# Optimization experiments

Measured on AMD Instinct MI355X. Metric: run time of the kernel, lower is better.

The kernel has to match this reference:

```python
import jax, jax.numpy as jnp
import numpy as np

EMBED = 768
HEADS = 12
HEAD_DIM = EMBED // HEADS
B, T = 2, 2048


def setup_inputs() -> dict:
    key = jax.random.key(0)
    ks = jax.random.split(key, 5)
    scale = 0.02
    return {
        "x": jax.random.normal(ks[0], (B, T, EMBED), dtype=jnp.float32),
        "Wq": jax.random.normal(ks[1], (HEADS, EMBED, HEAD_DIM), dtype=jnp.float32) * scale,
        "Wk": jax.random.normal(ks[2], (HEADS, EMBED, HEAD_DIM), dtype=jnp.float32) * scale,
        "Wv": jax.random.normal(ks[3], (HEADS, EMBED, HEAD_DIM), dtype=jnp.float32) * scale,
        "Wp": jax.random.normal(ks[4], (EMBED, EMBED), dtype=jnp.float32) * scale,
        "bp": jnp.zeros((EMBED,), dtype=jnp.float32),
    }


def reference(x, Wq, Wk, Wv, Wp, bp):
    # x: [B,T,E]; per-head projections batched over the head axis.
    q = jnp.einsum("bte,hed->bhtd", x, Wq)  # [B,H,T,Dh]
    k = jnp.einsum("bte,hed->bhtd", x, Wk)
    v = jnp.einsum("bte,hed->bhtd", x, Wv)
    scale = 1.0 / jnp.sqrt(jnp.asarray(HEAD_DIM, dtype=x.dtype))
    scores = jnp.einsum("bhtd,bhsd->bhts", q, k) * scale  # [B,H,T,T]
    Tlen = x.shape[1]
    causal = jnp.tril(jnp.ones((Tlen, Tlen), dtype=bool))
    scores = jnp.where(causal[None, None], scores, jnp.asarray(-jnp.inf, dtype=scores.dtype))
    attn = jax.nn.softmax(scores, axis=-1)
    out = jnp.einsum("bhts,bhsd->bhtd", attn, v)  # [B,H,T,Dh]
    # concat heads (same layout as torch.cat over per-head outputs)
    out = out.transpose(0, 2, 1, 3).reshape(x.shape[0], Tlen, HEADS * HEAD_DIM)
    return out @ Wp + bp
```

## Files before the change

### kernel.cpp

```cpp
#include <hip/hip_runtime.h>
#include <math.h>

namespace {

constexpr int E_  = 768;
constexpr int H_  = 12;
constexpr int DH_ = 64;
constexpr int T_  = 2048;
constexpr int B_  = 2;
constexpr int M_  = B_ * T_;

typedef __attribute__((ext_vector_type(8))) short bf16x8;
typedef __attribute__((ext_vector_type(4))) float f32x4;

__device__ inline ushort f2bf(float f) {
  union { float f; unsigned u; } v; v.f = f;
  unsigned u = v.u + 0x7FFFu + ((v.u >> 16) & 1u);
  return (ushort)(u >> 16);
}

__device__ __forceinline__ void gl16(const ushort* g, ushort* l) {
  __builtin_amdgcn_global_load_lds(
      (const __attribute__((address_space(1))) unsigned int*)(g),
      (__attribute__((address_space(3))) unsigned int*)(l), 16, 0, 0);
}

__global__ __launch_bounds__(256) void convert_x_k(
    const float* __restrict__ x, ushort* __restrict__ xb)
{
  const size_t i = ((size_t)blockIdx.x * 256 + threadIdx.x) * 8;
  float4 a = *(const float4*)(x + i);
  float4 b = *(const float4*)(x + i + 4);
  ushort o[8] = {f2bf(a.x), f2bf(a.y), f2bf(a.z), f2bf(a.w),
                 f2bf(b.x), f2bf(b.y), f2bf(b.z), f2bf(b.w)};
  *(bf16x8*)(xb + i) = *(bf16x8*)o;
}

__global__ __launch_bounds__(256) void transpose_w_k(
    const float* __restrict__ Wq, const float* __restrict__ Wk,
    const float* __restrict__ Wv, const float* __restrict__ Wp,
    ushort* __restrict__ Wt, ushort* __restrict__ Wpt)
{
  __shared__ float tile[64][65];
  const int bid = blockIdx.x;
  const int tid = threadIdx.x;
  const int tr = tid >> 4, tc = tid & 15;

  const float* src; ushort* dst;
  int k0, n0, sN, dK;
  if (bid < 432) {
    const int mat = bid / 144, rem = bid % 144;
    const int h = rem / 12, ktile = rem % 12;
    const float* W = (mat == 0) ? Wq : (mat == 1) ? Wk : Wv;
    src = W + (size_t)h * E_ * DH_;
    dst = Wt + (size_t)(mat * H_ + h) * DH_ * E_;
    k0 = ktile * 64; n0 = 0; sN = DH_; dK = E_;
  } else {
    const int rem = bid - 432;
    src = Wp;
    dst = Wpt;
    k0 = (rem / 12) * 64; n0 = (rem % 12) * 64; sN = E_; dK = E_;
  }

#pragma unroll
  for (int rr = 0; rr < 64; rr += 16) {
    float4 v = *(const float4*)(src + (size_t)(k0 + tr + rr) * sN + n0 + tc * 4);
    tile[tr + rr][tc * 4 + 0] = v.x;
    tile[tr + rr][tc * 4 + 1] = v.y;
    tile[tr + rr][tc * 4 + 2] = v.z;
    tile[tr + rr][tc * 4 + 3] = v.w;
  }
  __syncthreads();
#pragma unroll
  for (int rr = 0; rr < 64; rr += 16) {
    const int n = tr + rr;
    ushort4 o;
    o.x = f2bf(tile[tc * 4 + 0][n]);
    o.y = f2bf(tile[tc * 4 + 1][n]);
    o.z = f2bf(tile[tc * 4 + 2][n]);
    o.w = f2bf(tile[tc * 4 + 3][n]);
    *(ushort4*)(dst + (size_t)(n0 + n) * dK + k0 + tc * 4) = o;
  }
}

constexpr float QSCALE = 0.18033688f;

__global__ __launch_bounds__(256) void qkv_fused_k(
    const ushort* __restrict__ xb, const ushort* __restrict__ Wt,
    ushort* __restrict__ q_ws, ushort* __restrict__ k_ws, ushort* __restrict__ vt_ws)
{
  __shared__ __align__(16) ushort lds[2 * 128 * 64];
  ushort* As = lds;
  ushort* Bs = lds + 128 * 64;

  const int n0 = blockIdx.x * 128;
  const int m0 = blockIdx.y * 128;

  const int tid  = threadIdx.x;
  const int w    = tid >> 6, l = tid & 63;
  const int lrow = l & 15, lk = l >> 4;
  const int r7   = lrow & 7;

  const int srow = l >> 3;
  const int sch  = (l & 7) ^ srow;

  f32x4 acc[2][8] = {};

  for (int k0 = 0; k0 < E_; k0 += 64) {
#pragma unroll
    for (int r = 0; r < 4; ++r) {
      const int base = r * 32 + w * 8;
      gl16(xb + (size_t)(m0 + base + srow) * E_ + k0 + sch * 8, &As[base * 64]);
      gl16(Wt + (size_t)(n0 + base + srow) * E_ + k0 + sch * 8, &Bs[base * 64]);
    }
    __syncthreads();

#pragma unroll
    for (int kk = 0; kk < 2; ++kk) {
      const int cof = ((kk * 4 + lk) ^ r7) * 8;
      const bf16x8 a0 = *(const bf16x8*)&As[(w * 32 + lrow) * 64 + cof];
      const bf16x8 a1 = *(const bf16x8*)&As[(w * 32 + 16 + lrow) * 64 + cof];
#pragma unroll
      for (int nf = 0; nf < 8; ++nf) {
        const bf16x8 b = *(const bf16x8*)&Bs[(nf * 16 + lrow) * 64 + cof];
        acc[0][nf] = __builtin_amdgcn_mfma_f32_16x16x32_bf16(a0, b, acc[0][nf], 0, 0, 0);
        acc[1][nf] = __builtin_amdgcn_mfma_f32_16x16x32_bf16(a1, b, acc[1][nf], 0, 0, 0);
      }
    }
    __syncthreads();
  }

  const int b  = m0 >> 11;
  const int t0 = m0 & 2047;
  ushort* Td = lds;

#pragma unroll
  for (int half = 0; half < 2; ++half) {
    const int seg = (n0 >> 6) + half;
    const int mat = seg / H_;
    const int h   = seg - mat * H_;
    const int bh  = b * H_ + h;

    if (mat != 2) {
      const float qs = (mat == 0) ? QSCALE : 1.0f;
      ushort* outw = (mat == 0) ? q_ws : k_ws;
#pragma unroll
      for (int mi = 0; mi < 2; ++mi)
#pragma unroll
        for (int i = 0; i < 4; ++i) {
          const int t = t0 + w * 32 + mi * 16 + lk * 4 + i;
          ushort* orow = outw + ((size_t)bh * T_ + t) * DH_;
#pragma unroll
          for (int nf2 = 0; nf2 < 4; ++nf2)
            orow[nf2 * 16 + lrow] = f2bf(acc[mi][half * 4 + nf2][i] * qs);
        }
    } else {
      __syncthreads();
#pragma unroll
      for (int mi = 0; mi < 2; ++mi)
#pragma unroll
        for (int i = 0; i < 4; ++i) {
          const int tl = w * 32 + mi * 16 + lk * 4 + i;
#pragma unroll
          for (int nf2 = 0; nf2 < 4; ++nf2)
            Td[(nf2 * 16 + lrow) * 136 + tl] = f2bf(acc[mi][half * 4 + nf2][i]);
        }
      __syncthreads();
#pragma unroll
      for (int it = 0; it < 4; ++it) {
        const int c = tid + it * 256;
        const int d = c >> 4, sub = c & 15;
        *(bf16x8*)(vt_ws + ((size_t)bh * DH_ + d) * T_ + t0 + sub * 8) =
            *(const bf16x8*)&Td[d * 136 + sub * 8];
      }
    }
  }
}

__global__ __launch_bounds__(256) void attn_mfma_k(
    const ushort* __restrict__ q_ws, const ushort* __restrict__ k_ws,
    const ushort* __restrict__ vt_ws, ushort* __restrict__ o_ws)
{
  __shared__ __align__(16) ushort Ks[2][64 * 64];
  __shared__ __align__(16) ushort Vt[2][64 * 64];
  __shared__ __align__(16) ushort Pl[4][16 * 64];

  const int qt = 31 - (int)blockIdx.y;
  const int bh = blockIdx.x;
  const int q0 = qt * 64;
  const ushort* Qb  = q_ws + (size_t)bh * T_ * DH_;
  const ushort* Kb  = k_ws + (size_t)bh * T_ * DH_;
  const ushort* VTb = vt_ws + (size_t)bh * DH_ * T_;

  const int tid  = threadIdx.x;
  const int w    = tid >> 6;
  const int l    = tid & 63;
  const int lrow = l & 15;
  const int lk   = l >> 4;
  const int r7   = lrow & 7;
  const int rr   = tid >> 3;
  const int sub  = tid & 7;
  const int swc  = sub ^ (rr & 7);

  const int st0 = rr * 64 + swc * 8;
  const int st1 = (rr + 32) * 64 + swc * 8;

  int kof0[4], kof1[4];
#pragma unroll
  for (int ct = 0; ct < 4; ++ct) {
    kof0[ct] = (ct * 16 + lrow) * 64 + ((lk ^ r7) * 8);
    kof1[ct] = (ct * 16 + lrow) * 64 + (((lk + 4) ^ r7) * 8);
  }

  const ushort* Qrow = Qb + (size_t)(q0 + w * 16 + lrow) * DH_;
  const bf16x8 qa0 = *(const bf16x8*)(Qrow + lk * 8);
  const bf16x8 qa1 = *(const bf16x8*)(Qrow + lk * 8 + 32);
  const int qglob = q0 + w * 16 + lrow;

  float m_r = -INFINITY, l_r = 0.f;
  f32x4 oc[4] = {};

  ushort* Pw = &Pl[w][0];
  const int rd0 = lrow * 64 + ((lk ^ r7) * 8);
  const int rd1 = lrow * 64 + (((lk + 4) ^ r7) * 8);
  const int wrbase  = lrow * 128 + (lk & 1) * 8;
  const int wrchunk = (lk >> 1);

  bf16x8 kp0 = *(const bf16x8*)(Kb + (size_t)rr * DH_ + sub * 8);
  bf16x8 kp1 = *(const bf16x8*)(Kb + (size_t)(rr + 32) * DH_ + sub * 8);
  bf16x8 vp0 = *(const bf16x8*)(VTb + (size_t)rr * T_ + sub * 8);
  bf16x8 vp1 = *(const bf16x8*)(VTb + (size_t)(rr + 32) * T_ + sub * 8);
  *(bf16x8*)&Ks[0][st0] = kp0;
  *(bf16x8*)&Ks[0][st1] = kp1;
  *(bf16x8*)&Vt[0][st0] = vp0;
  *(bf16x8*)&Vt[0][st1] = vp1;
  __syncthreads();

  for (int kt = 0; kt <= qt; ++kt) {
    const int s0  = kt * 64;
    const int cur = kt & 1;

    if (kt < qt) {
      const int sn = s0 + 64;
      kp0 = *(const bf16x8*)(Kb + (size_t)(sn + rr) * DH_ + sub * 8);
      kp1 = *(const bf16x8*)(Kb + (size_t)(sn + rr + 32) * DH_ + sub * 8);
      vp0 = *(const bf16x8*)(VTb + (size_t)rr * T_ + sn + sub * 8);
      vp1 = *(const bf16x8*)(VTb + (size_t)(rr + 32) * T_ + sn + sub * 8);
    }

    f32x4 st[4];
#pragma unroll
    for (int ct = 0; ct < 4; ++ct) {
      const bf16x8 kb0 = *(const bf16x8*)&Ks[cur][kof0[ct]];
      const bf16x8 kb1 = *(const bf16x8*)&Ks[cur][kof1[ct]];
      f32x4 z = {0.f, 0.f, 0.f, 0.f};
      z = __builtin_amdgcn_mfma_f32_16x16x32_bf16(kb0, qa0, z, 0, 0, 0);
      st[ct] = __builtin_amdgcn_mfma_f32_16x16x32_bf16(kb1, qa1, z, 0, 0, 0);
    }

    if (kt == qt) {
#pragma unroll
      for (int ct = 0; ct < 4; ++ct)
#pragma unroll
        for (int i = 0; i < 4; ++i)
          if (s0 + ct * 16 + lk * 4 + i > qglob) st[ct][i] = -INFINITY;
    }

    float mc[4];
#pragma unroll
    for (int ct = 0; ct < 4; ++ct)
      mc[ct] = fmaxf(fmaxf(st[ct][0], st[ct][1]), fmaxf(st[ct][2], st[ct][3]));
    float mx = fmaxf(fmaxf(mc[0], mc[1]), fmaxf(mc[2], mc[3]));
    mx = fmaxf(mx, __shfl_xor(mx, 16));
    mx = fmaxf(mx, __shfl_xor(mx, 32));

    if (__any(mx > m_r + 8.f)) {
      const float mn   = fmaxf(m_r, mx);
      const float corr = exp2f(m_r - mn);
      m_r = mn;
      l_r *= corr;
#pragma unroll
      for (int i = 0; i < 4; ++i) {
        const float cr = __shfl(corr, lk * 4 + i);
#pragma unroll
        for (int ct = 0; ct < 4; ++ct) oc[ct][i] *= cr;
      }
    }

    float sc[4];
#pragma unroll
    for (int ct = 0; ct < 4; ++ct) {
#pragma unroll
      for (int i = 0; i < 4; ++i) st[ct][i] = exp2f(st[ct][i] - m_r);
      sc[ct] = (st[ct][0] + st[ct][1]) + (st[ct][2] + st[ct][3]);
    }
    float rs = (sc[0] + sc[1]) + (sc[2] + sc[3]);
    rs += __shfl_xor(rs, 16);
    rs += __shfl_xor(rs, 32);
    l_r += rs;

#pragma unroll
    for (int ct = 0; ct < 4; ++ct) {
      unsigned lo, hi;
      asm("v_cvt_pk_bf16_f32 %0, %1, %2" : "=v"(lo) : "v"(st[ct][0]), "v"(st[ct][1]));
      asm("v_cvt_pk_bf16_f32 %0, %1, %2" : "=v"(hi) : "v"(st[ct][2]), "v"(st[ct][3]));
      uint2 pk; pk.x = lo; pk.y = hi;
      const int ch = ((ct * 2 + wrchunk) ^ r7);
      *(uint2*)((char*)Pw + wrbase + ch * 16) = pk;
    }

    const bf16x8 pa0 = *(const bf16x8*)(Pw + rd0);
    const bf16x8 pa1 = *(const bf16x8*)(Pw + rd1);

#pragma unroll
    for (int ct = 0; ct < 4; ++ct) {
      const bf16x8 vb0 = *(const bf16x8*)&Vt[cur][kof0[ct]];
      const bf16x8 vb1 = *(const bf16x8*)&Vt[cur][kof1[ct]];
      oc[ct] = __builtin_amdgcn_mfma_f32_16x16x32_bf16(pa0, vb0, oc[ct], 0, 0, 0);
      oc[ct] = __builtin_amdgcn_mfma_f32_16x16x32_bf16(pa1, vb1, oc[ct], 0, 0, 0);
    }

    if (kt < qt) {
      const int nxt = cur ^ 1;
      *(bf16x8*)&Ks[nxt][st0] = kp0;
      *(bf16x8*)&Ks[nxt][st1] = kp1;
      *(bf16x8*)&Vt[nxt][st0] = vp0;
      *(bf16x8*)&Vt[nxt][st1] = vp1;
    }
    __syncthreads();
  }

  const int bb = bh / H_, hh = bh - (bh / H_) * H_;
#pragma unroll
  for (int i = 0; i < 4; ++i) {
    const float lv  = __shfl(l_r, lk * 4 + i);
    const float inv = 1.0f / lv;
    const int t = q0 + w * 16 + lk * 4 + i;
    ushort* orow = o_ws + ((size_t)bb * T_ + t) * E_ + hh * DH_;
#pragma unroll
    for (int ct = 0; ct < 4; ++ct)
      orow[ct * 16 + lrow] = f2bf(oc[ct][i] * inv);
  }
}

__global__ __launch_bounds__(256) void proj2_k(
    const ushort* __restrict__ ob, const ushort* __restrict__ Wpt,
    const float* __restrict__ bp, float* __restrict__ out)
{
  __shared__ __align__(16) ushort lds[2 * 128 * 64];
  ushort* As = lds;
  ushort* Bs = lds + 128 * 64;

  const int n0 = blockIdx.x * 128;
  const int m0 = blockIdx.y * 128;

  const int tid  = threadIdx.x;
  const int w    = tid >> 6, l = tid & 63;
  const int lrow = l & 15, lk = l >> 4;
  const int r7   = lrow & 7;
  const int srow = l >> 3;
  const int sch  = (l & 7) ^ srow;

  f32x4 acc[2][8] = {};

  for (int k0 = 0; k0 < E_; k0 += 64) {
#pragma unroll
    for (int r = 0; r < 4; ++r) {
      const int base = r * 32 + w * 8;
      gl16(ob  + (size_t)(m0 + base + srow) * E_ + k0 + sch * 8, &As[base * 64]);
      gl16(Wpt + (size_t)(n0 + base + srow) * E_ + k0 + sch * 8, &Bs[base * 64]);
    }
    __syncthreads();

#pragma unroll
    for (int kk = 0; kk < 2; ++kk) {
      const int cof = ((kk * 4 + lk) ^ r7) * 8;
      const bf16x8 a0 = *(const bf16x8*)&As[(w * 32 + lrow) * 64 + cof];
      const bf16x8 a1 = *(const bf16x8*)&As[(w * 32 + 16 + lrow) * 64 + cof];
#pragma unroll
      for (int nf = 0; nf < 8; ++nf) {
        const bf16x8 b = *(const bf16x8*)&Bs[(nf * 16 + lrow) * 64 + cof];
        acc[0][nf] = __builtin_amdgcn_mfma_f32_16x16x32_bf16(a0, b, acc[0][nf], 0, 0, 0);
        acc[1][nf] = __builtin_amdgcn_mfma_f32_16x16x32_bf16(a1, b, acc[1][nf], 0, 0, 0);
      }
    }
    __syncthreads();
  }

  float bias[8];
#pragma unroll
  for (int nf = 0; nf < 8; ++nf) bias[nf] = bp[n0 + nf * 16 + lrow];

#pragma unroll
  for (int mi = 0; mi < 2; ++mi)
#pragma unroll
    for (int i = 0; i < 4; ++i) {
      const int m = m0 + w * 32 + mi * 16 + lk * 4 + i;
      float* orow = out + (size_t)m * E_ + n0;
#pragma unroll
      for (int nf = 0; nf < 8; ++nf)
        orow[nf * 16 + lrow] = acc[mi][nf][i] + bias[nf];
    }
}

}

extern "C" void kernel_launch(void* const* d_in, const int* in_sizes, int n_in,
                              void* d_out, int out_size, void* d_ws, size_t ws_size,
                              hipStream_t stream) {
  const float* x  = (const float*)d_in[0];
  const float* Wq = (const float*)d_in[1];
  const float* Wk = (const float*)d_in[2];
  const float* Wv = (const float*)d_in[3];
  const float* Wp = (const float*)d_in[4];
  const float* bp = (const float*)d_in[5];
  float* out = (float*)d_out;

  const size_t nx  = (size_t)M_ * E_;
  const size_t nwt = (size_t)3 * H_ * DH_ * E_;
  const size_t nwp = (size_t)E_ * E_;
  const size_t per = (size_t)B_ * H_ * T_ * DH_;

  ushort* xb    = (ushort*)d_ws;
  ushort* Wt    = xb + nx;
  ushort* Wpt   = Wt + nwt;
  ushort* q_ws  = Wpt + nwp;
  ushort* k_ws  = q_ws + per;
  ushort* vt_ws = k_ws + per;
  ushort* o_b   = vt_ws + per;

  convert_x_k<<<dim3((int)(nx / (256 * 8))), 256, 0, stream>>>(x, xb);
  transpose_w_k<<<dim3(576), 256, 0, stream>>>(Wq, Wk, Wv, Wp, Wt, Wpt);
  qkv_fused_k<<<dim3(18, 32), 256, 0, stream>>>(xb, Wt, q_ws, k_ws, vt_ws);
  attn_mfma_k<<<dim3(24, 32), 256, 0, stream>>>(q_ws, k_ws, vt_ws, o_b);
  proj2_k<<<dim3(6, 32), 256, 0, stream>>>(o_b, Wpt, bp, out);
}
```

Measured before the change: 110.6 us.

## Split attention KV range across two blocks and add combine kernel

The attention kernel gains a grid z-dimension of two, so each query tile's causal key range is split in half and processed by two blocks. Each block writes unnormalised bf16 partial outputs plus the running max and sum, and a new combine kernel merges them with log-sum-exp weights. K/V shared memory drops from double to single buffering, and the x conversion and weight transpose kernels are merged into one launch. The goal is more parallelism and less tail imbalance from the causal triangle, at the cost of an extra kernel launch, extra global traffic for the partials, and bf16 rounding of the partials.

```diff
diff --git a/kernel.cpp b/kernel.cpp
--- a/kernel.cpp
+++ b/kernel.cpp
@@ -9,6 +9,7 @@
 constexpr int T_  = 2048;
 constexpr int B_  = 2;
 constexpr int M_  = B_ * T_;
+constexpr int BH_ = B_ * H_;
 
 typedef __attribute__((ext_vector_type(8))) short bf16x8;
 typedef __attribute__((ext_vector_type(4))) float f32x4;
@@ -18,6 +19,9 @@
   unsigned u = v.u + 0x7FFFu + ((v.u >> 16) & 1u);
   return (ushort)(u >> 16);
 }
+__device__ inline float bf2f(ushort u) {
+  union { unsigned u; float f; } v; v.u = (unsigned)u << 16; return v.f;
+}
 
 __device__ __forceinline__ void gl16(const ushort* g, ushort* l) {
   __builtin_amdgcn_global_load_lds(
@@ -25,38 +29,41 @@
       (__attribute__((address_space(3))) unsigned int*)(l), 16, 0, 0);
 }
 
-__global__ __launch_bounds__(256) void convert_x_k(
-    const float* __restrict__ x, ushort* __restrict__ xb)
-{
-  const size_t i = ((size_t)blockIdx.x * 256 + threadIdx.x) * 8;
-  float4 a = *(const float4*)(x + i);
-  float4 b = *(const float4*)(x + i + 4);
-  ushort o[8] = {f2bf(a.x), f2bf(a.y), f2bf(a.z), f2bf(a.w),
-                 f2bf(b.x), f2bf(b.y), f2bf(b.z), f2bf(b.w)};
-  *(bf16x8*)(xb + i) = *(bf16x8*)o;
-}
-
-__global__ __launch_bounds__(256) void transpose_w_k(
+constexpr int NCONV = 1536;
+
+__global__ __launch_bounds__(256) void prep_k(
+    const float* __restrict__ x,
     const float* __restrict__ Wq, const float* __restrict__ Wk,
     const float* __restrict__ Wv, const float* __restrict__ Wp,
-    ushort* __restrict__ Wt, ushort* __restrict__ Wpt)
+    ushort* __restrict__ xb, ushort* __restrict__ Wt, ushort* __restrict__ Wpt)
 {
   __shared__ float tile[64][65];
   const int bid = blockIdx.x;
   const int tid = threadIdx.x;
+
+  if (bid < NCONV) {
+    const size_t i = ((size_t)bid * 256 + tid) * 8;
+    float4 a = *(const float4*)(x + i);
+    float4 b = *(const float4*)(x + i + 4);
+    ushort o[8] = {f2bf(a.x), f2bf(a.y), f2bf(a.z), f2bf(a.w),
+                   f2bf(b.x), f2bf(b.y), f2bf(b.z), f2bf(b.w)};
+    *(bf16x8*)(xb + i) = *(bf16x8*)o;
+    return;
+  }
+
+  const int wb = bid - NCONV;
   const int tr = tid >> 4, tc = tid & 15;
-
   const float* src; ushort* dst;
   int k0, n0, sN, dK;
-  if (bid < 432) {
-    const int mat = bid / 144, rem = bid % 144;
+  if (wb < 432) {
+    const int mat = wb / 144, rem = wb % 144;
     const int h = rem / 12, ktile = rem % 12;
     const float* W = (mat == 0) ? Wq : (mat == 1) ? Wk : Wv;
     src = W + (size_t)h * E_ * DH_;
     dst = Wt + (size_t)(mat * H_ + h) * DH_ * E_;
     k0 = ktile * 64; n0 = 0; sN = DH_; dK = E_;
   } else {
-    const int rem = bid - 432;
+    const int rem = wb - 432;
     src = Wp;
     dst = Wpt;
     k0 = (rem / 12) * 64; n0 = (rem % 12) * 64; sN = E_; dK = E_;
@@ -100,7 +107,6 @@
   const int w    = tid >> 6, l = tid & 63;
   const int lrow = l & 15, lk = l >> 4;
   const int r7   = lrow & 7;
-
   const int srow = l >> 3;
   const int sch  = (l & 7) ^ srow;
 
@@ -177,17 +183,23 @@
   }
 }
 
-__global__ __launch_bounds__(256) void attn_mfma_k(
+__global__ __launch_bounds__(256) void attn_split_k(
     const ushort* __restrict__ q_ws, const ushort* __restrict__ k_ws,
-    const ushort* __restrict__ vt_ws, ushort* __restrict__ o_ws)
+    const ushort* __restrict__ vt_ws, ushort* __restrict__ op_ws,
+    float2* __restrict__ ml_ws)
 {
-  __shared__ __align__(16) ushort Ks[2][64 * 64];
-  __shared__ __align__(16) ushort Vt[2][64 * 64];
+  __shared__ __align__(16) ushort Ks[64 * 64];
+  __shared__ __align__(16) ushort Vt[64 * 64];
   __shared__ __align__(16) ushort Pl[4][16 * 64];
 
   const int qt = 31 - (int)blockIdx.y;
   const int bh = blockIdx.x;
+  const int hz = blockIdx.z;
+  const int nt = qt + 1;
+  const int klo = hz ? (nt >> 1) : 0;
+  const int khi = hz ? nt : (nt >> 1);
   const int q0 = qt * 64;
+
   const ushort* Qb  = q_ws + (size_t)bh * T_ * DH_;
   const ushort* Kb  = k_ws + (size_t)bh * T_ * DH_;
   const ushort* VTb = vt_ws + (size_t)bh * DH_ * T_;
@@ -226,121 +238,151 @@
   const int wrbase  = lrow * 128 + (lk & 1) * 8;
   const int wrchunk = (lk >> 1);
 
-  bf16x8 kp0 = *(const bf16x8*)(Kb + (size_t)rr * DH_ + sub * 8);
-  bf16x8 kp1 = *(const bf16x8*)(Kb + (size_t)(rr + 32) * DH_ + sub * 8);
-  bf16x8 vp0 = *(const bf16x8*)(VTb + (size_t)rr * T_ + sub * 8);
-  bf16x8 vp1 = *(const bf16x8*)(VTb + (size_t)(rr + 32) * T_ + sub * 8);
-  *(bf16x8*)&Ks[0][st0] = kp0;
-  *(bf16x8*)&Ks[0][st1] = kp1;
-  *(bf16x8*)&Vt[0][st0] = vp0;
-  *(bf16x8*)&Vt[0][st1] = vp1;
-  __syncthreads();
-
-  for (int kt = 0; kt <= qt; ++kt) {
-    const int s0  = kt * 64;
-    const int cur = kt & 1;
-
-    if (kt < qt) {
-      const int sn = s0 + 64;
-      kp0 = *(const bf16x8*)(Kb + (size_t)(sn + rr) * DH_ + sub * 8);
-      kp1 = *(const bf16x8*)(Kb + (size_t)(sn + rr + 32) * DH_ + sub * 8);
-      vp0 = *(const bf16x8*)(VTb + (size_t)rr * T_ + sn + sub * 8);
-      vp1 = *(const bf16x8*)(VTb + (size_t)(rr + 32) * T_ + sn + sub * 8);
-    }
-
-    f32x4 st[4];
-#pragma unroll
-    for (int ct = 0; ct < 4; ++ct) {
-      const bf16x8 kb0 = *(const bf16x8*)&Ks[cur][kof0[ct]];
-      const bf16x8 kb1 = *(const bf16x8*)&Ks[cur][kof1[ct]];
-      f32x4 z = {0.f, 0.f, 0.f, 0.f};
-      z = __builtin_amdgcn_mfma_f32_16x16x32_bf16(kb0, qa0, z, 0, 0, 0);
-      st[ct] = __builtin_amdgcn_mfma_f32_16x16x32_bf16(kb1, qa1, z, 0, 0, 0);
-    }
-
-    if (kt == qt) {
+  if (klo < khi) {
+    bf16x8 kp0 = *(const bf16x8*)(Kb + (size_t)(klo * 64 + rr) * DH_ + sub * 8);
+    bf16x8 kp1 = *(const bf16x8*)(Kb + (size_t)(klo * 64 + rr + 32) * DH_ + sub * 8);
+    bf16x8 vp0 = *(const bf16x8*)(VTb + (size_t)rr * T_ + klo * 64 + sub * 8);
+    bf16x8 vp1 = *(const bf16x8*)(VTb + (size_t)(rr + 32) * T_ + klo * 64 + sub * 8);
+
+    for (int kt = klo; kt < khi; ++kt) {
+      const int s0 = kt * 64;
+
+      *(bf16x8*)&Ks[st0] = kp0;
+      *(bf16x8*)&Ks[st1] = kp1;
+      *(bf16x8*)&Vt[st0] = vp0;
+      *(bf16x8*)&Vt[st1] = vp1;
+      __syncthreads();
+
+      if (kt + 1 < khi) {
+        const int sn = s0 + 64;
+        kp0 = *(const bf16x8*)(Kb + (size_t)(sn + rr) * DH_ + sub * 8);
+        kp1 = *(const bf16x8*)(Kb + (size_t)(sn + rr + 32) * DH_ + sub * 8);
+        vp0 = *(const bf16x8*)(VTb + (size_t)rr * T_ + sn + sub * 8);
+        vp1 = *(const bf16x8*)(VTb + (size_t)(rr + 32) * T_ + sn + sub * 8);
+      }
+
+      f32x4 st[4];
+#pragma unroll
+      for (int ct = 0; ct < 4; ++ct) {
+        const bf16x8 kb0 = *(const bf16x8*)&Ks[kof0[ct]];
+        const bf16x8 kb1 = *(const bf16x8*)&Ks[kof1[ct]];
+        f32x4 z = {0.f, 0.f, 0.f, 0.f};
+        z = __builtin_amdgcn_mfma_f32_16x16x32_bf16(kb0, qa0, z, 0, 0, 0);
+        st[ct] = __builtin_amdgcn_mfma_f32_16x16x32_bf16(kb1, qa1, z, 0, 0, 0);
+      }
+
+      if (kt == qt) {
+#pragma unroll
+        for (int ct = 0; ct < 4; ++ct)
+#pragma unroll
+          for (int i = 0; i < 4; ++i)
+            if (s0 + ct * 16 + lk * 4 + i > qglob) st[ct][i] = -INFINITY;
+      }
+
+      float mc[4];
 #pragma unroll
       for (int ct = 0; ct < 4; ++ct)
-#pragma unroll
-        for (int i = 0; i < 4; ++i)
-          if (s0 + ct * 16 + lk * 4 + i > qglob) st[ct][i] = -INFINITY;
-    }
-
-    float mc[4];
+        mc[ct] = fmaxf(fmaxf(st[ct][0], st[ct][1]), fmaxf(st[ct][2], st[ct][3]));
+      float mx = fmaxf(fmaxf(mc[0], mc[1]), fmaxf(mc[2], mc[3]));
+      mx = fmaxf(mx, __shfl_xor(mx, 16));
+      mx = fmaxf(mx, __shfl_xor(mx, 32));
+
+      if (__any(mx > m_r + 8.f)) {
+        const float mn   = fmaxf(m_r, mx);
+        const float corr = exp2f(m_r - mn);
+        m_r = mn;
+        l_r *= corr;
+#pragma unroll
+        for (int i = 0; i < 4; ++i) {
+          const float cr = __shfl(corr, lk * 4 + i);
+#pragma unroll
+          for (int ct = 0; ct < 4; ++ct) oc[ct][i] *= cr;
+        }
+      }
+
+      float sc[4];
+#pragma unroll
+      for (int ct = 0; ct < 4; ++ct) {
+#pragma unroll
+        for (int i = 0; i < 4; ++i) st[ct][i] = exp2f(st[ct][i] - m_r);
+        sc[ct] = (st[ct][0] + st[ct][1]) + (st[ct][2] + st[ct][3]);
+      }
+      float rs = (sc[0] + sc[1]) + (sc[2] + sc[3]);
+      rs += __shfl_xor(rs, 16);
+      rs += __shfl_xor(rs, 32);
+      l_r += rs;
+
+#pragma unroll
+      for (int ct = 0; ct < 4; ++ct) {
+        unsigned lo, hi;
+        asm("v_cvt_pk_bf16_f32 %0, %1, %2" : "=v"(lo) : "v"(st[ct][0]), "v"(st[ct][1]));
+        asm("v_cvt_pk_bf16_f32 %0, %1, %2" : "=v"(hi) : "v"(st[ct][2]), "v"(st[ct][3]));
+        uint2 pk; pk.x = lo; pk.y = hi;
+        const int ch = ((ct * 2 + wrchunk) ^ r7);
+        *(uint2*)((char*)Pw + wrbase + ch * 16) = pk;
+      }
+
+      const bf16x8 pa0 = *(const bf16x8*)(Pw + rd0);
+      const bf16x8 pa1 = *(const bf16x8*)(Pw + rd1);
+
+#pragma unroll
+      for (int ct = 0; ct < 4; ++ct) {
+        const bf16x8 vb0 = *(const bf16x8*)&Vt[kof0[ct]];
+        const bf16x8 vb1 = *(const bf16x8*)&Vt[kof1[ct]];
+        oc[ct] = __builtin_amdgcn_mfma_f32_16x16x32_bf16(pa0, vb0, oc[ct], 0, 0, 0);
+        oc[ct] = __builtin_amdgcn_mfma_f32_16x16x32_bf16(pa1, vb1, oc[ct], 0, 0, 0);
+      }
+      __syncthreads();
+    }
+  }
+
+  const size_t pb = (size_t)(hz * BH_ + bh) * T_;
+  if (lk == 0)
+    ml_ws[pb + q0 + w * 16 + lrow] = make_float2(m_r, l_r);
+#pragma unroll
+  for (int i = 0; i < 4; ++i) {
+    const int t = q0 + w * 16 + lk * 4 + i;
+    ushort* orow = op_ws + (pb + t) * DH_;
 #pragma unroll
     for (int ct = 0; ct < 4; ++ct)
-      mc[ct] = fmaxf(fmaxf(st[ct][0], st[ct][1]), fmaxf(st[ct][2], st[ct][3]));
-    float mx = fmaxf(fmaxf(mc[0], mc[1]), fmaxf(mc[2], mc[3]));
-    mx = fmaxf(mx, __shfl_xor(mx, 16));
-    mx = fmaxf(mx, __shfl_xor(mx, 32));
-
-    if (__any(mx > m_r + 8.f)) {
-      const float mn   = fmaxf(m_r, mx);
-      const float corr = exp2f(m_r - mn);
-      m_r = mn;
-      l_r *= corr;
-#pragma unroll
-      for (int i = 0; i < 4; ++i) {
-        const float cr = __shfl(corr, lk * 4 + i);
-#pragma unroll
-        for (int ct = 0; ct < 4; ++ct) oc[ct][i] *= cr;
-      }
-    }
-
-    float sc[4];
-#pragma unroll
-    for (int ct = 0; ct < 4; ++ct) {
-#pragma unroll
-      for (int i = 0; i < 4; ++i) st[ct][i] = exp2f(st[ct][i] - m_r);
-      sc[ct] = (st[ct][0] + st[ct][1]) + (st[ct][2] + st[ct][3]);
-    }
-    float rs = (sc[0] + sc[1]) + (sc[2] + sc[3]);
-    rs += __shfl_xor(rs, 16);
-    rs += __shfl_xor(rs, 32);
-    l_r += rs;
-
-#pragma unroll
-    for (int ct = 0; ct < 4; ++ct) {
-      unsigned lo, hi;
-      asm("v_cvt_pk_bf16_f32 %0, %1, %2" : "=v"(lo) : "v"(st[ct][0]), "v"(st[ct][1]));
-      asm("v_cvt_pk_bf16_f32 %0, %1, %2" : "=v"(hi) : "v"(st[ct][2]), "v"(st[ct][3]));
-      uint2 pk; pk.x = lo; pk.y = hi;
-      const int ch = ((ct * 2 + wrchunk) ^ r7);
-      *(uint2*)((char*)Pw + wrbase + ch * 16) = pk;
-    }
-
-    const bf16x8 pa0 = *(const bf16x8*)(Pw + rd0);
-    const bf16x8 pa1 = *(const bf16x8*)(Pw + rd1);
-
-#pragma unroll
-    for (int ct = 0; ct < 4; ++ct) {
-      const bf16x8 vb0 = *(const bf16x8*)&Vt[cur][kof0[ct]];
-      const bf16x8 vb1 = *(const bf16x8*)&Vt[cur][kof1[ct]];
-      oc[ct] = __builtin_amdgcn_mfma_f32_16x16x32_bf16(pa0, vb0, oc[ct], 0, 0, 0);
-      oc[ct] = __builtin_amdgcn_mfma_f32_16x16x32_bf16(pa1, vb1, oc[ct], 0, 0, 0);
-    }
-
-    if (kt < qt) {
-      const int nxt = cur ^ 1;
-      *(bf16x8*)&Ks[nxt][st0] = kp0;
-      *(bf16x8*)&Ks[nxt][st1] = kp1;
-      *(bf16x8*)&Vt[nxt][st0] = vp0;
-      *(bf16x8*)&Vt[nxt][st1] = vp1;
-    }
-    __syncthreads();
-  }
-
+      orow[ct * 16 + lrow] = f2bf(oc[ct][i]);
+  }
+}
+
+__global__ __launch_bounds__(256) void attn_combine_k(
+    const ushort* __restrict__ op_ws, const float2* __restrict__ ml_ws,
+    ushort* __restrict__ o_ws)
+{
+  const int bh = blockIdx.x;
+  const int t  = blockIdx.y * 64 + (threadIdx.x >> 2);
+  const int d0 = (threadIdx.x & 3) * 16;
+
+  const size_t ixA = (size_t)bh * T_ + t;
+  const size_t ixB = (size_t)(BH_ + bh) * T_ + t;
+  const float2 mlA = ml_ws[ixA];
+  const float2 mlB = ml_ws[ixB];
+  const float m   = fmaxf(mlA.x, mlB.x);
+  const float wA  = exp2f(mlA.x - m);
+  const float wB  = exp2f(mlB.x - m);
+  const float inv = 1.0f / (wA * mlA.y + wB * mlB.y);
+
+  const ushort* pA = op_ws + ixA * DH_ + d0;
+  const ushort* pB = op_ws + ixB * DH_ + d0;
+  bf16x8 a0 = *(const bf16x8*)pA;
+  bf16x8 a1 = *(const bf16x8*)(pA + 8);
+  bf16x8 b0 = *(const bf16x8*)pB;
+  bf16x8 b1 = *(const bf16x8*)(pB + 8);
+
+  ushort o[16];
+#pragma unroll
+  for (int j = 0; j < 8; ++j) {
+    o[j]     = f2bf((wA * bf2f((ushort)a0[j]) + wB * bf2f((ushort)b0[j])) * inv);
+    o[8 + j] = f2bf((wA * bf2f((ushort)a1[j]) + wB * bf2f((ushort)b1[j])) * inv);
+  }
   const int bb = bh / H_, hh = bh - (bh / H_) * H_;
-#pragma unroll
-  for (int i = 0; i < 4; ++i) {
-    const float lv  = __shfl(l_r, lk * 4 + i);
-    const float inv = 1.0f / lv;
-    const int t = q0 + w * 16 + lk * 4 + i;
-    ushort* orow = o_ws + ((size_t)bb * T_ + t) * E_ + hh * DH_;
-#pragma unroll
-    for (int ct = 0; ct < 4; ++ct)
-      orow[ct * 16 + lrow] = f2bf(oc[ct][i] * inv);
-  }
+  ushort* po = o_ws + ((size_t)bb * T_ + t) * E_ + hh * DH_ + d0;
+  *(bf16x8*)po       = *(const bf16x8*)&o[0];
+  *(bf16x8*)(po + 8) = *(const bf16x8*)&o[8];
 }
 
 __global__ __launch_bounds__(256) void proj2_k(
@@ -419,7 +461,7 @@
   const size_t nx  = (size_t)M_ * E_;
   const size_t nwt = (size_t)3 * H_ * DH_ * E_;
   const size_t nwp = (size_t)E_ * E_;
-  const size_t per = (size_t)B_ * H_ * T_ * DH_;
+  const size_t per = (size_t)BH_ * T_ * DH_;
 
   ushort* xb    = (ushort*)d_ws;
   ushort* Wt    = xb + nx;
@@ -428,10 +470,12 @@
   ushort* k_ws  = q_ws + per;
   ushort* vt_ws = k_ws + per;
   ushort* o_b   = vt_ws + per;
-
-  convert_x_k<<<dim3((int)(nx / (256 * 8))), 256, 0, stream>>>(x, xb);
-  transpose_w_k<<<dim3(576), 256, 0, stream>>>(Wq, Wk, Wv, Wp, Wt, Wpt);
+  ushort* op_ws = o_b + per;
+  float2* ml_ws = (float2*)(op_ws + 2 * per);
+
+  prep_k<<<dim3(NCONV + 576), 256, 0, stream>>>(x, Wq, Wk, Wv, Wp, xb, Wt, Wpt);
   qkv_fused_k<<<dim3(18, 32), 256, 0, stream>>>(xb, Wt, q_ws, k_ws, vt_ws);
-  attn_mfma_k<<<dim3(24, 32), 256, 0, stream>>>(q_ws, k_ws, vt_ws, o_b);
+  attn_split_k<<<dim3(24, 32, 2), 256, 0, stream>>>(q_ws, k_ws, vt_ws, op_ws, ml_ws);
+  attn_combine_k<<<dim3(24, 32), 256, 0, stream>>>(op_ws, ml_ws, o_b);
   proj2_k<<<dim3(6, 32), 256, 0, stream>>>(o_b, Wpt, bp, out);
 }
```

After: 102.3 us. 1.08x faster.
